# Performance work log

Hardware: AMD Instinct MI355X
Metric: run time of the kernel (lower is better)

## Reference

```python
import jax, jax.numpy as jnp
import numpy as np

NQ = 8  # qubits per circuit (= d_k = n_qubits_ffn)
# Fixed realization of tq.RandomLayer(n_ops=8): 6 parametric rotations + 2 CNOTs
OPS = [("ry", 0), ("rx", 3), ("rz", 5), ("cx", (1, 4)), ("ry", 6), ("rx", 2), ("cx", (0, 7)), ("rz", 4)]
_CNOT = jnp.asarray(np.array([[1,0,0,0],[0,1,0,0],[0,0,0,1],[0,0,1,0]], dtype=np.complex64).reshape(2,2,2,2))
# signs[i, w] = +1 if bit of wire w in basis index i is 0, else -1 (PauliZ eigenvalue)
_idx = np.arange(2 ** NQ)
_bits = (_idx[:, None] >> (NQ - 1 - np.arange(NQ))) & 1
SIGNS = jnp.asarray((1 - 2 * _bits).astype(np.float32))

def _rot(kind, t):
    c = jnp.cos(t / 2).astype(jnp.complex64)
    s = jnp.sin(t / 2).astype(jnp.complex64)
    z = jnp.zeros_like(c)
    if kind == "rx":
        return jnp.stack([jnp.stack([c, -1j * s]), jnp.stack([-1j * s, c])])
    if kind == "ry":
        return jnp.stack([jnp.stack([c, -s]), jnp.stack([s, c])])
    tc = t.astype(jnp.complex64)
    return jnp.stack([jnp.stack([jnp.exp(-1j * tc / 2), z]), jnp.stack([z, jnp.exp(1j * tc / 2)])])

def _apply1(state, U, w):
    st = jnp.tensordot(U, state, axes=((1,), (w + 1,)))
    return jnp.moveaxis(st, 0, w + 1)

def _apply2(state, c, t):  # CNOT, requires c < t (true for OPS)
    st = jnp.tensordot(_CNOT, state, axes=((2, 3), (c + 1, t + 1)))
    return jnp.moveaxis(st, (0, 1), (c + 1, t + 1))

def qcircuit(angles, thetas):
    """angles: [N, NQ] data angles (RX encoding); thetas: [6] gate params.
    Returns PauliZ expectations [N, NQ] (float32)."""
    N = angles.shape[0]
    c = jnp.cos(angles / 2)
    s = jnp.sin(angles / 2)
    amp = jnp.stack([c.astype(jnp.complex64), (-1j) * s.astype(jnp.complex64)], axis=-1)  # [N, NQ, 2]
    # RX-encoded product state |psi> = prod_w RX(x_w)|0>
    state = amp[:, 0]
    for w in range(1, NQ):
        state = state[..., None] * amp[:, w].reshape((N,) + (1,) * w + (2,))
    pi = 0
    for kind, arg in OPS:
        if kind == "cx":
            state = _apply2(state, *arg)
        else:
            state = _apply1(state, _rot(kind, thetas[pi]), arg)
            pi += 1
    probs = jnp.abs(state.reshape(N, -1)) ** 2  # [N, 2^NQ]
    return probs @ SIGNS  # [N, NQ]

def _ln(x, g, b, eps=1e-5):
    m = x.mean(-1, keepdims=True)
    v = ((x - m) ** 2).mean(-1, keepdims=True)
    return (x - m) / jnp.sqrt(v + eps) * g + b

def setup_inputs() -> dict:
    key = jax.random.key(0)
    ks = jax.random.split(key, 8)
    B, S, E, FF = 4, 1024, 64, 256
    return {
        "x": jax.random.normal(ks[0], (B, S, E), dtype=jnp.float32),
        "attn_theta": jax.random.uniform(ks[1], (6,), dtype=jnp.float32, maxval=2 * np.pi),
        "Wc": jax.random.normal(ks[2], (E, E), dtype=jnp.float32) * 0.1,
        "bc": jnp.zeros((E,), jnp.float32),
        "g1": jnp.ones((E,), jnp.float32),
        "beta1": jnp.zeros((E,), jnp.float32),
        "ffn_theta": jax.random.uniform(ks[3], (6,), dtype=jnp.float32, maxval=2 * np.pi),
        "W1": jax.random.normal(ks[4], (NQ, FF), dtype=jnp.float32) * 0.3,
        "b1": jnp.zeros((FF,), jnp.float32),
        "W2": jax.random.normal(ks[5], (FF, E), dtype=jnp.float32) * 0.06,
        "b2": jnp.zeros((E,), jnp.float32),
        "g2": jnp.ones((E,), jnp.float32),
        "beta2": jnp.zeros((E,), jnp.float32),
    }

def reference(x, attn_theta, Wc, bc, g1, beta1, ffn_theta, W1, b1, W2, b2, g2, beta2):
    B, S, E = x.shape
    dk = NQ  # d_k = embed_dim // num_heads = 8
    # --- quantum multi-head attention (same qlayer shared across heads -> vectorize) ---
    q = qcircuit(x.reshape(B * S * (E // dk), dk), attn_theta)  # [B*S*H, dk]
    attn = q.reshape(B, S, E) @ Wc + bc
    y = _ln(x + attn, g1, beta1)
    # --- quantum FFN: encoder uses first NQ features of each token ---
    qf = qcircuit(y.reshape(B * S, E)[:, :NQ], ffn_theta)  # [B*S, NQ]
    h = jax.nn.relu(qf @ W1 + b1)
    ffn = (h @ W2 + b2).reshape(B, S, E)
    return _ln(y + ffn, g2, beta2)
```

## Files before the change

kernel.cpp:

```cpp
#include <hip/hip_runtime.h>


typedef _Float16 h2f   __attribute__((ext_vector_type(2)));
typedef _Float16 f16x8 __attribute__((ext_vector_type(8)));
typedef float    f32x4 __attribute__((ext_vector_type(4)));
typedef int      i32x4 __attribute__((ext_vector_type(4)));

__device__ __forceinline__ int pk(float a, float b) {
    return __builtin_bit_cast(int, __builtin_amdgcn_cvt_pkrtz(a, b));
}
__device__ __forceinline__ float fdot2i(int a, int b, float c) {
    return __builtin_amdgcn_fdot2(__builtin_bit_cast(h2f, a),
                                  __builtin_bit_cast(h2f, b), c, false);
}
__device__ __forceinline__ float rl_f(float v, int l) {
    return __int_as_float(__builtin_amdgcn_readlane(__float_as_int(v), l));
}
__device__ __forceinline__ f16x8 pack8(const float (&v)[8]) {
    i32x4 p;
    p.x = pk(v[0], v[1]);
    p.y = pk(v[2], v[3]);
    p.z = pk(v[4], v[5]);
    p.w = pk(v[6], v[7]);
    return __builtin_bit_cast(f16x8, p);
}
__device__ __forceinline__ void wave_sum4(float& a, float& b, float& c, float& d) {
#pragma unroll
    for (int m = 32; m > 0; m >>= 1) {
        a += __shfl_xor(a, m, 64);
        b += __shfl_xor(b, m, 64);
        c += __shfl_xor(c, m, 64);
        d += __shfl_xor(d, m, 64);
    }
}

__global__ __launch_bounds__(256, 2)
void qtb_fused12(const float* __restrict__ x,
                 const float* __restrict__ th_a,
                 const float* __restrict__ Wc,
                 const float* __restrict__ bc,
                 const float* __restrict__ g1,
                 const float* __restrict__ be1,
                 const float* __restrict__ th_f,
                 const float* __restrict__ W1,
                 const float* __restrict__ b1,
                 const float* __restrict__ W2,
                 const float* __restrict__ b2,
                 const float* __restrict__ g2,
                 const float* __restrict__ be2,
                 float* __restrict__ out)
{
    __shared__ __align__(16) int4      sW1[256];
    __shared__ __align__(16) _Float16  sZ[16][72];
    __shared__ __align__(16) float     sA[16][66];
    __shared__ __align__(16) _Float16  sH[16][264];
    __shared__ __align__(16) float     sO[16][66];

    const int tid  = threadIdx.x;
    const int lane = tid & 63;
    const int wv   = tid >> 6;
    const int w    = lane & 7;
    const int gb   = lane & ~7;
    const int tok0 = (blockIdx.x * 4 + wv) * 2;
    const int tl   = wv * 2;
    const int col  = lane & 15;
    const int kg   = lane >> 4;

    float xr[2];
#pragma unroll
    for (int t = 0; t < 2; ++t) xr[t] = x[(tok0 + t) * 64 + lane];

    float bfa[2][8];
    float bff[8][8];
    {
        const float* base = Wc + wv * 16 + col;
#pragma unroll
        for (int ks = 0; ks < 2; ++ks)
#pragma unroll
            for (int i = 0; i < 8; ++i)
                bfa[ks][i] = base[(ks * 32 + kg * 8 + i) * 64];
    }
    {
        const float* base = W2 + wv * 16 + col;
#pragma unroll
        for (int ks = 0; ks < 8; ++ks)
#pragma unroll
            for (int i = 0; i < 8; ++i)
                bff[ks][i] = base[(ks * 32 + kg * 8 + i) * 64];
    }

    if (tid < 64) {
        int j0 = tid * 4;
        float4 r[8];
#pragma unroll
        for (int k = 0; k < 8; ++k) r[k] = *(const float4*)&W1[k * 256 + j0];
        const float* f = (const float*)r;
#pragma unroll
        for (int j = 0; j < 4; ++j)
            sW1[j0 + j] = make_int4(pk(f[0 * 4 + j], f[4 * 4 + j]),
                                    pk(f[1 * 4 + j], f[5 * 4 + j]),
                                    pk(f[2 * 4 + j], f[6 * 4 + j]),
                                    pk(f[3 * 4 + j], f[7 * 4 + j]));
    }

    const float C0a = __cosf(th_a[0]);
    const float T1a = th_a[1];
    const float C3a = __cosf(th_a[3]);
    const float T4a = th_a[4];
    const float C0f = __cosf(th_f[0]);
    const float T1f = th_f[1];
    const float C3f = __cosf(th_f[3]);
    const float T4f = th_f[4];

    const float bcL = bc[lane], g1L = g1[lane], be1L = be1[lane];
    const float b2L = b2[lane], g2L = g2[lane], be2L = be2[lane];
    float b1L[4];
#pragma unroll
    for (int r = 0; r < 4; ++r) b1L[r] = b1[r * 64 + lane];

    const float dA = (w == 2) ? T4a : ((w == 3) ? T1a : 0.0f);
#pragma unroll
    for (int t = 0; t < 2; ++t) {
        float c  = __cosf(xr[t] + dA);
        float c0 = __shfl(c, gb, 64);
        float c1 = __shfl(c, gb + 1, 64);
        float zz = c * ((w == 0) ? C0a : ((w == 6) ? C3a : 1.0f));
        if (w == 4) zz = c * c1;
        if (w == 7) zz = C0a * c0 * c;
        sZ[tl + t][lane] = (_Float16)zz;
    }

    f16x8 bfragA[2], bfragF[8];
#pragma unroll
    for (int ks = 0; ks < 2; ++ks) bfragA[ks] = pack8(bfa[ks]);
#pragma unroll
    for (int ks = 0; ks < 8; ++ks) bfragF[ks] = pack8(bff[ks]);

    __syncthreads();

    {
        f32x4 cacc = {0.0f, 0.0f, 0.0f, 0.0f};
#pragma unroll
        for (int ks = 0; ks < 2; ++ks) {
            f16x8 af = *(const f16x8*)&sZ[col][ks * 32 + kg * 8];
            cacc = __builtin_amdgcn_mfma_f32_16x16x32_f16(af, bfragA[ks], cacc, 0, 0, 0);
        }
#pragma unroll
        for (int r = 0; r < 4; ++r)
            sA[kg * 4 + r][wv * 16 + col] = cacc[r];
    }

    __syncthreads();

    float y[2];
    {
        float v0 = xr[0] + sA[tl + 0][lane] + bcL;
        float v1 = xr[1] + sA[tl + 1][lane] + bcL;
        float s0 = v0, q0 = v0 * v0, s1 = v1, q1 = v1 * v1;
        wave_sum4(s0, q0, s1, q1);
        float m0 = s0 * 0.015625f, m1 = s1 * 0.015625f;
        float r0 = rsqrtf(q0 * 0.015625f - m0 * m0 + 1e-5f);
        float r1 = rsqrtf(q1 * 0.015625f - m1 * m1 + 1e-5f);
        y[0] = (v0 - m0) * r0 * g1L + be1L;
        y[1] = (v1 - m1) * r1 * g1L + be1L;
    }

    int4 w1q[4];
#pragma unroll
    for (int r = 0; r < 4; ++r) w1q[r] = sW1[r * 64 + lane];

    const float dF = (w == 2) ? T4f : ((w == 3) ? T1f : 0.0f);
#pragma unroll
    for (int t = 0; t < 2; ++t) {
        float cy = __cosf(y[t] + dF);
        float c0 = rl_f(cy, 0);
        float c1 = rl_f(cy, 1);
        float qz = cy * ((w == 0) ? C0f : ((w == 6) ? C3f : 1.0f));
        if (w == 4) qz = cy * c1;
        if (w == 7) qz = C0f * c0 * cy;
        int qp0 = pk(rl_f(qz, 0), rl_f(qz, 4));
        int qp1 = pk(rl_f(qz, 1), rl_f(qz, 5));
        int qp2 = pk(rl_f(qz, 2), rl_f(qz, 6));
        int qp3 = pk(rl_f(qz, 3), rl_f(qz, 7));
#pragma unroll
        for (int r = 0; r < 4; ++r) {
            float a = b1L[r];
            a = fdot2i(qp0, w1q[r].x, a);
            a = fdot2i(qp1, w1q[r].y, a);
            a = fdot2i(qp2, w1q[r].z, a);
            a = fdot2i(qp3, w1q[r].w, a);
            sH[tl + t][r * 64 + lane] = (_Float16)fmaxf(a, 0.0f);
        }
    }

    __syncthreads();

    {
        f32x4 cacc = {0.0f, 0.0f, 0.0f, 0.0f};
#pragma unroll
        for (int ks = 0; ks < 8; ++ks) {
            f16x8 af = *(const f16x8*)&sH[col][ks * 32 + kg * 8];
            cacc = __builtin_amdgcn_mfma_f32_16x16x32_f16(af, bfragF[ks], cacc, 0, 0, 0);
        }
#pragma unroll
        for (int r = 0; r < 4; ++r)
            sO[kg * 4 + r][wv * 16 + col] = cacc[r];
    }

    __syncthreads();

    {
        float v0 = y[0] + b2L + sO[tl + 0][lane];
        float v1 = y[1] + b2L + sO[tl + 1][lane];
        float s0 = v0, q0 = v0 * v0, s1 = v1, q1 = v1 * v1;
        wave_sum4(s0, q0, s1, q1);
        float m0 = s0 * 0.015625f, m1 = s1 * 0.015625f;
        float r0 = rsqrtf(q0 * 0.015625f - m0 * m0 + 1e-5f);
        float r1 = rsqrtf(q1 * 0.015625f - m1 * m1 + 1e-5f);
        out[(tok0 + 0) * 64 + lane] = (v0 - m0) * r0 * g2L + be2L;
        out[(tok0 + 1) * 64 + lane] = (v1 - m1) * r1 * g2L + be2L;
    }
}

extern "C" void kernel_launch(void* const* d_in, const int* in_sizes, int n_in,
                              void* d_out, int out_size, void* d_ws, size_t ws_size,
                              hipStream_t stream)
{
    const float* x   = (const float*)d_in[0];
    const float* at  = (const float*)d_in[1];
    const float* Wc  = (const float*)d_in[2];
    const float* bcp = (const float*)d_in[3];
    const float* g1  = (const float*)d_in[4];
    const float* be1 = (const float*)d_in[5];
    const float* ft  = (const float*)d_in[6];
    const float* W1  = (const float*)d_in[7];
    const float* b1  = (const float*)d_in[8];
    const float* W2  = (const float*)d_in[9];
    const float* b2  = (const float*)d_in[10];
    const float* g2  = (const float*)d_in[11];
    const float* be2 = (const float*)d_in[12];
    float* out = (float*)d_out;

    qtb_fused12<<<512, 256, 0, stream>>>(x, at, Wc, bcp, g1, be1, ft,
                                         W1, b1, W2, b2, g2, be2, out);
}
```

Baseline: 10.38 us.

## Split MFMA stages across specialised waves in 512-thread blocks

Doubles the block to 8 waves (16 tokens per block, half the blocks). The first four waves hold only the Wc fragments and do the attention projection MFMA, and the last four hold only the W2 fragments and do the FFN output MFMA. This roughly halves per-wave B-fragment register pressure and global weight loads per token. It also splits each accumulation chain into two independent accumulators and raises wave priority around the MFMAs. In exchange, each MFMA phase leaves half the waves idle, and the larger block may change occupancy.

```diff
diff --git a/kernel.cpp b/kernel.cpp
--- a/kernel.cpp
+++ b/kernel.cpp
@@ -34,8 +34,8 @@
     }
 }
 
-__global__ __launch_bounds__(256, 2)
-void qtb_fused12(const float* __restrict__ x,
+__global__ __launch_bounds__(512, 2)
+void qtb_fused13(const float* __restrict__ x,
                  const float* __restrict__ th_a,
                  const float* __restrict__ Wc,
                  const float* __restrict__ bc,
@@ -61,7 +61,7 @@
     const int wv   = tid >> 6;
     const int w    = lane & 7;
     const int gb   = lane & ~7;
-    const int tok0 = (blockIdx.x * 4 + wv) * 2;
+    const int tok0 = (blockIdx.x * 8 + wv) * 2;
     const int tl   = wv * 2;
     const int col  = lane & 15;
     const int kg   = lane >> 4;
@@ -72,16 +72,15 @@
 
     float bfa[2][8];
     float bff[8][8];
-    {
+    if (wv < 4) {
         const float* base = Wc + wv * 16 + col;
 #pragma unroll
         for (int ks = 0; ks < 2; ++ks)
 #pragma unroll
             for (int i = 0; i < 8; ++i)
                 bfa[ks][i] = base[(ks * 32 + kg * 8 + i) * 64];
-    }
-    {
-        const float* base = W2 + wv * 16 + col;
+    } else {
+        const float* base = W2 + (wv - 4) * 16 + col;
 #pragma unroll
         for (int ks = 0; ks < 8; ++ks)
 #pragma unroll
@@ -89,8 +88,8 @@
                 bff[ks][i] = base[(ks * 32 + kg * 8 + i) * 64];
     }
 
-    if (tid < 64) {
-        int j0 = tid * 4;
+    if (tid >= 64 && tid < 128) {
+        int j0 = (tid - 64) * 4;
         float4 r[8];
 #pragma unroll
         for (int k = 0; k < 8; ++k) r[k] = *(const float4*)&W1[k * 256 + j0];
@@ -130,24 +129,29 @@
         sZ[tl + t][lane] = (_Float16)zz;
     }
 
-    f16x8 bfragA[2], bfragF[8];
-#pragma unroll
-    for (int ks = 0; ks < 2; ++ks) bfragA[ks] = pack8(bfa[ks]);
-#pragma unroll
-    for (int ks = 0; ks < 8; ++ks) bfragF[ks] = pack8(bff[ks]);
-
-    __syncthreads();
-
-    {
-        f32x4 cacc = {0.0f, 0.0f, 0.0f, 0.0f};
-#pragma unroll
-        for (int ks = 0; ks < 2; ++ks) {
-            f16x8 af = *(const f16x8*)&sZ[col][ks * 32 + kg * 8];
-            cacc = __builtin_amdgcn_mfma_f32_16x16x32_f16(af, bfragA[ks], cacc, 0, 0, 0);
-        }
+    f16x8 bfrag[8];
+    if (wv < 4) {
+#pragma unroll
+        for (int ks = 0; ks < 2; ++ks) bfrag[ks] = pack8(bfa[ks]);
+    } else {
+#pragma unroll
+        for (int ks = 0; ks < 8; ++ks) bfrag[ks] = pack8(bff[ks]);
+    }
+
+    __syncthreads();
+
+    if (wv < 4) {
+        __builtin_amdgcn_s_setprio(1);
+        f16x8 af0 = *(const f16x8*)&sZ[col][0 * 32 + kg * 8];
+        f16x8 af1 = *(const f16x8*)&sZ[col][1 * 32 + kg * 8];
+        f32x4 c0 = {0.0f, 0.0f, 0.0f, 0.0f};
+        f32x4 c1 = {0.0f, 0.0f, 0.0f, 0.0f};
+        c0 = __builtin_amdgcn_mfma_f32_16x16x32_f16(af0, bfrag[0], c0, 0, 0, 0);
+        c1 = __builtin_amdgcn_mfma_f32_16x16x32_f16(af1, bfrag[1], c1, 0, 0, 0);
+        __builtin_amdgcn_s_setprio(0);
 #pragma unroll
         for (int r = 0; r < 4; ++r)
-            sA[kg * 4 + r][wv * 16 + col] = cacc[r];
+            sA[kg * 4 + r][wv * 16 + col] = c0[r] + c1[r];
     }
 
     __syncthreads();
@@ -195,16 +199,21 @@
 
     __syncthreads();
 
-    {
-        f32x4 cacc = {0.0f, 0.0f, 0.0f, 0.0f};
-#pragma unroll
-        for (int ks = 0; ks < 8; ++ks) {
-            f16x8 af = *(const f16x8*)&sH[col][ks * 32 + kg * 8];
-            cacc = __builtin_amdgcn_mfma_f32_16x16x32_f16(af, bfragF[ks], cacc, 0, 0, 0);
+    if (wv >= 4) {
+        __builtin_amdgcn_s_setprio(1);
+        f32x4 c0 = {0.0f, 0.0f, 0.0f, 0.0f};
+        f32x4 c1 = {0.0f, 0.0f, 0.0f, 0.0f};
+#pragma unroll
+        for (int ks = 0; ks < 8; ks += 2) {
+            f16x8 af0 = *(const f16x8*)&sH[col][(ks    ) * 32 + kg * 8];
+            f16x8 af1 = *(const f16x8*)&sH[col][(ks + 1) * 32 + kg * 8];
+            c0 = __builtin_amdgcn_mfma_f32_16x16x32_f16(af0, bfrag[ks    ], c0, 0, 0, 0);
+            c1 = __builtin_amdgcn_mfma_f32_16x16x32_f16(af1, bfrag[ks + 1], c1, 0, 0, 0);
         }
+        __builtin_amdgcn_s_setprio(0);
 #pragma unroll
         for (int r = 0; r < 4; ++r)
-            sO[kg * 4 + r][wv * 16 + col] = cacc[r];
+            sO[kg * 4 + r][(wv - 4) * 16 + col] = c0[r] + c1[r];
     }
 
     __syncthreads();
@@ -241,6 +250,6 @@
     const float* be2 = (const float*)d_in[12];
     float* out = (float*)d_out;
 
-    qtb_fused12<<<512, 256, 0, stream>>>(x, at, Wc, bcp, g1, be1, ft,
+    qtb_fused13<<<256, 512, 0, stream>>>(x, at, Wc, bcp, g1, be1, ft,
                                          W1, b1, W2, b2, g2, be2, out);
 }
```

After: 9.882 us. -4.8%, faster.
